# Kernel tuning notes

Measured on AMD Instinct MI355X. Metric: run time of the kernel, lower is better.

The kernel has to match this reference:

```python
import jax, jax.numpy as jnp
import numpy as np

B, Q, C, G = 16, 2000, 80, 100
COST_CLASS, COST_BBOX, COST_GIOU = 2.0, 5.0, 2.0
ALPHA, GAMMA = 0.25, 2.0
OTA_K = 5
CENTER_RADIUS = 2.5
MAX_ITERS = 1000  # safety cap on the (normally rarely-entered) rescue while-loop


def cxcywh_to_xyxy(b):
    cx, cy, w, h = jnp.split(b, 4, axis=-1)
    return jnp.concatenate([cx - 0.5 * w, cy - 0.5 * h, cx + 0.5 * w, cy + 0.5 * h], -1)


def xyxy_to_cxcywh(b):
    x1, y1, x2, y2 = jnp.split(b, 4, axis=-1)
    return jnp.concatenate([(x1 + x2) * 0.5, (y1 + y2) * 0.5, x2 - x1, y2 - y1], -1)


def box_iou(a, b):
    # a: [Q,4], b: [G,4] xyxy -> iou [Q,G], union [Q,G]
    area_a = (a[:, 2] - a[:, 0]) * (a[:, 3] - a[:, 1])
    area_b = (b[:, 2] - b[:, 0]) * (b[:, 3] - b[:, 1])
    lt = jnp.maximum(a[:, None, :2], b[None, :, :2])
    rb = jnp.minimum(a[:, None, 2:], b[None, :, 2:])
    wh = jnp.clip(rb - lt, 0.0)
    inter = wh[..., 0] * wh[..., 1]
    union = area_a[:, None] + area_b[None, :] - inter
    return inter / union, union


def generalized_box_iou(a, b):
    iou, union = box_iou(a, b)
    lt = jnp.minimum(a[:, None, :2], b[None, :, :2])
    rb = jnp.maximum(a[:, None, 2:], b[None, :, 2:])
    wh = jnp.clip(rb - lt, 0.0)
    area = wh[..., 0] * wh[..., 1]
    return iou - (area - union) / area


def get_in_boxes_info(boxes_c, tgt_c):
    # boxes_c: [Q,4] cxcywh (abs), tgt_c: [G,4] cxcywh (abs)
    xy = cxcywh_to_xyxy(tgt_c)  # [G,4]
    ax = boxes_c[:, 0:1]  # [Q,1]
    ay = boxes_c[:, 1:2]
    in_box = (ax > xy[:, 0][None, :]) & (ax < xy[:, 2][None, :]) & \
             (ay > xy[:, 1][None, :]) & (ay < xy[:, 3][None, :])  # [Q,G]
    w = xy[:, 2] - xy[:, 0]
    h = xy[:, 3] - xy[:, 1]
    in_ctr = (ax > (tgt_c[:, 0] - CENTER_RADIUS * w)[None, :]) & \
             (ax < (tgt_c[:, 0] + CENTER_RADIUS * w)[None, :]) & \
             (ay > (tgt_c[:, 1] - CENTER_RADIUS * h)[None, :]) & \
             (ay < (tgt_c[:, 1] + CENTER_RADIUS * h)[None, :])
    fg_mask = in_box.any(1) | in_ctr.any(1)  # [Q]
    return fg_mask, in_box & in_ctr


def dynamic_k_matching(cost, ious):
    # cost, ious: [Q,G]
    topk_ious, _ = jax.lax.top_k(ious.T, OTA_K)  # [G,k]
    dyn_k = jnp.clip(topk_ious.sum(1).astype(jnp.int32), 1, None)  # [G], <= OTA_K
    # rank of each query within each gt column (ascending cost, stable ties)
    ranks = jnp.argsort(jnp.argsort(cost, axis=0), axis=0)
    M = (ranks < dyn_k[None, :]).astype(cost.dtype)  # topk(largest=False) per column

    onehot = lambda idx: jax.nn.one_hot(idx, G, dtype=cost.dtype)
    # resolve anchors matched to >1 gt: keep the min-cost gt
    conflict0 = M.sum(1) > 1  # stale mask reused inside the while loop (faithful to torch code)
    M = jnp.where(conflict0[:, None], onehot(jnp.argmin(cost, axis=1)), M)

    qidx = jnp.arange(Q)

    def cond(state):
        M, cost, it = state
        return ((M.sum(0) == 0).any()) & (it < MAX_ITERS)

    def body(state):
        M, cost, it = state
        matched = M.sum(1) > 0
        cost = cost + 100000.0 * matched[:, None].astype(cost.dtype)
        unmatched_gt = M.sum(0) == 0  # [G]
        pos = jnp.argmin(cost, axis=0)  # [G] best anchor per gt (same cost for all, as in torch)
        add = unmatched_gt[None, :] & (qidx[:, None] == pos[None, :])
        M = jnp.where(add, jnp.asarray(1.0, cost.dtype), M)
        has_conf = (M.sum(1) > 1).any()
        M = jnp.where((has_conf & conflict0)[:, None], onehot(jnp.argmin(cost, axis=1)), M)
        return M, cost, it + 1

    M, cost, _ = jax.lax.while_loop(cond, body, (M, cost, jnp.int32(0)))

    selected = M.sum(1) > 0  # [Q] bool
    gt_idx = jnp.argmax(M, axis=1).astype(jnp.int32)  # [Q] (valid where selected)
    cost_m = jnp.where(M == 0, jnp.asarray(1e30, cost.dtype), cost)
    matched_qid = jnp.argmin(cost_m, axis=0).astype(jnp.int32)  # [G]
    return selected, gt_idx, matched_qid, M


def _match_one(logits, boxes, gtb, labels, img):
    # logits [Q,C], boxes [Q,4] cxcywh, gtb [G,4] cxcywh norm, labels [G] int, img [4]
    prob = jax.nn.sigmoid(logits)
    boxes_abs = cxcywh_to_xyxy(boxes) * img
    gt_abs = cxcywh_to_xyxy(gtb) * img
    fg_mask, in_bc = get_in_boxes_info(xyxy_to_cxcywh(boxes_abs), xyxy_to_cxcywh(gt_abs))
    ious, _ = box_iou(boxes_abs, gt_abs)
    neg = (1.0 - ALPHA) * prob ** GAMMA * (-jnp.log(1.0 - prob + 1e-8))
    pos = ALPHA * (1.0 - prob) ** GAMMA * (-jnp.log(prob + 1e-8))
    cost_class = (pos - neg)[:, labels]  # [Q,G]
    cost_bbox = jnp.sum(jnp.abs(boxes_abs[:, None, :] / img - gt_abs[None, :, :] / img), -1)
    cost_giou = -generalized_box_iou(boxes_abs, gt_abs)
    cost = (COST_BBOX * cost_bbox + COST_CLASS * cost_class + COST_GIOU * cost_giou
            + 100.0 * (~in_bc).astype(cost_bbox.dtype)
            + 10000.0 * (~fg_mask)[:, None].astype(cost_bbox.dtype))
    return dynamic_k_matching(cost, ious)


def setup_inputs() -> dict:
    key = jax.random.key(0)
    k1, k2, k3, k4 = jax.random.split(key, 4)
    return {
        "pred_logits": jax.random.normal(k1, (B, Q, C), dtype=jnp.float32),
        "pred_boxes": jax.random.uniform(k2, (B, Q, 4), dtype=jnp.float32),
        "gt_boxes": jax.random.uniform(k3, (B, G, 4), dtype=jnp.float32),
        "labels": jax.random.randint(k4, (B, G), 0, C),
        "image_size_xyxy": jnp.ones((B, 4), dtype=jnp.float32),
    }


def reference(pred_logits, pred_boxes, gt_boxes, labels, image_size_xyxy):
    selected, gt_idx, matched_qid, M = jax.vmap(_match_one)(
        pred_logits, pred_boxes, gt_boxes, labels, image_size_xyxy)
    # selected [B,Q] bool, gt_idx [B,Q] int32, matched_qid [B,G] int32, M [B,Q,G] float
    return selected, gt_idx, matched_qid, M
```

## Files before the change

kernel.cpp:

```cpp
#include <hip/hip_runtime.h>
#include <stdint.h>

#define BATCH 16
#define NQ 2000
#define NC 80
#define NG 100
#define MAX_ITERS 1000
#define MAXC 96
#define QT 32
#define TILES 63
#define K1_BLOCKS (BATCH * TILES)
#define K3_BS 1024
#define NW3 16
#define NCAND 8
#define LSTRIDE 9
#define QINF 0x7fffffff
#define SQINF 0x7fff

#define OFF_SEL 0
#define OFF_GTI (BATCH * NQ)
#define OFF_MQ (2 * BATCH * NQ)
#define OFF_M (2 * BATCH * NQ + BATCH * NG)

#define WS_LISTS 0
#define WS_MW    65536
#define WS_MIT   (WS_MW + 512000)
#define WS_CIDX  (WS_MIT + 64000)
#define WS_CROW  (WS_CIDX + 64000)
#define WS_SCAL  (WS_CROW + 614400)
#define WS_NEED  (WS_SCAL + 512)

__device__ __forceinline__ float fmut(float c, int k) {
    for (int i = 0; i < k; ++i) c += 100000.0f;
    return c;
}

__device__ __forceinline__ bool lexlt(float v1, int i1, float v2, int i2) {
    return (v1 < v2) | ((v1 == v2) & (i1 < i2));
}

#define CE(vv, ii, a, b) do { \
    bool t_ = lexlt(vv[b], ii[b], vv[a], ii[a]); \
    float lo_ = t_ ? vv[b] : vv[a]; float hi_ = t_ ? vv[a] : vv[b]; \
    int loi_ = t_ ? ii[b] : ii[a]; int hii_ = t_ ? ii[a] : ii[b]; \
    vv[a] = lo_; vv[b] = hi_; ii[a] = loi_; ii[b] = hii_; \
} while (0)

#define INS8(vv, ii, val, idx) do { float v_ = (val); int i_ = (idx); \
    bool ins_ = lexlt(v_, i_, vv[7], ii[7]); \
    vv[7] = ins_ ? v_ : vv[7]; ii[7] = ins_ ? i_ : ii[7]; \
    CE(vv, ii, 6, 7); CE(vv, ii, 5, 6); CE(vv, ii, 4, 5); CE(vv, ii, 3, 4); \
    CE(vv, ii, 2, 3); CE(vv, ii, 1, 2); CE(vv, ii, 0, 1); \
} while (0)

#define MERGE8(va, ia) do { \
    for (int off_ = 1; off_ < 64; off_ <<= 1) { \
        float bv_[8]; int bi_[8]; \
        _Pragma("unroll") \
        for (int j_ = 0; j_ < 8; ++j_) { bv_[j_] = __shfl_xor(va[j_], off_, 64); bi_[j_] = __shfl_xor(ia[j_], off_, 64); } \
        float mv_[8]; int mi_[8]; \
        _Pragma("unroll") \
        for (int j_ = 0; j_ < 8; ++j_) { \
            bool t_ = lexlt(bv_[7 - j_], bi_[7 - j_], va[j_], ia[j_]); \
            mv_[j_] = t_ ? bv_[7 - j_] : va[j_]; mi_[j_] = t_ ? bi_[7 - j_] : ia[j_]; \
        } \
        _Pragma("unroll") \
        for (int d_ = 4; d_ >= 1; d_ >>= 1) { \
            _Pragma("unroll") \
            for (int i_ = 0; i_ < 8; ++i_) { \
                if ((i_ & d_) == 0) CE(mv_, mi_, i_, (i_ | d_)); \
            } \
        } \
        _Pragma("unroll") \
        for (int j_ = 0; j_ < 8; ++j_) { va[j_] = mv_[j_]; ia[j_] = mi_[j_]; } \
    } \
} while (0)

__global__ __launch_bounds__(256) void fgcost_kernel(
    const float* __restrict__ logits, const float* __restrict__ pred_boxes,
    const float* __restrict__ gt_boxes, const int* __restrict__ labels,
    const float* __restrict__ img_sz, float* __restrict__ costT_all,
    float* __restrict__ rowamin) {
    const int tid = threadIdx.x;
    const int b = blockIdx.x / TILES;
    const int tile = blockIdx.x - b * TILES;
    const int q0 = tile * QT;

    __shared__ float ct[QT][NG + 1];
    __shared__ float s_rx1[NG], s_ry1[NG], s_rx2[NG], s_ry2[NG];
    __shared__ float s_clx[NG], s_chx[NG], s_cly[NG], s_chy[NG];
    __shared__ float s_gx1[NG], s_gy1[NG], s_gx2[NG], s_gy2[NG];
    __shared__ float s_d1[NG], s_d2[NG], s_d3[NG], s_d4[NG];
    __shared__ float s_ga[NG];
    __shared__ int s_lab[NG];
    __shared__ float pbx[QT][11];
    __shared__ unsigned fgm[QT];

    const float i0 = img_sz[b * 4 + 0], i1 = img_sz[b * 4 + 1];
    const float i2 = img_sz[b * 4 + 2], i3 = img_sz[b * 4 + 3];

    if (tid < NG) {
        const float4 gt = *reinterpret_cast<const float4*>(gt_boxes + (b * NG + tid) * 4);
        float GX1 = (gt.x - 0.5f * gt.z) * i0, GY1 = (gt.y - 0.5f * gt.w) * i1;
        float GX2 = (gt.x + 0.5f * gt.z) * i2, GY2 = (gt.y + 0.5f * gt.w) * i3;
        float tcx = (GX1 + GX2) * 0.5f, tcy = (GY1 + GY2) * 0.5f;
        float tw = GX2 - GX1, th = GY2 - GY1;
        float X1 = tcx - 0.5f * tw, Y1 = tcy - 0.5f * th;
        float X2 = tcx + 0.5f * tw, Y2 = tcy + 0.5f * th;
        float w_ = X2 - X1, h_ = Y2 - Y1;
        s_rx1[tid] = X1; s_ry1[tid] = Y1; s_rx2[tid] = X2; s_ry2[tid] = Y2;
        s_clx[tid] = tcx - 2.5f * w_; s_chx[tid] = tcx + 2.5f * w_;
        s_cly[tid] = tcy - 2.5f * h_; s_chy[tid] = tcy + 2.5f * h_;
        s_gx1[tid] = GX1; s_gy1[tid] = GY1; s_gx2[tid] = GX2; s_gy2[tid] = GY2;
        s_d1[tid] = GX1 / i0; s_d2[tid] = GY1 / i1; s_d3[tid] = GX2 / i2; s_d4[tid] = GY2 / i3;
        s_ga[tid] = (GX2 - GX1) * (GY2 - GY1);
        s_lab[tid] = labels[b * NG + tid];
    }
    if (tid < QT) {
        fgm[tid] = 0;
        int q = q0 + tid;
        if (q < NQ) {
            const float4 pb = *reinterpret_cast<const float4*>(pred_boxes + (size_t)(b * NQ + q) * 4);
            float x1 = (pb.x - 0.5f * pb.z) * i0, y1 = (pb.y - 0.5f * pb.w) * i1;
            float x2 = (pb.x + 0.5f * pb.z) * i2, y2 = (pb.y + 0.5f * pb.w) * i3;
            pbx[tid][0] = x1; pbx[tid][1] = y1; pbx[tid][2] = x2; pbx[tid][3] = y2;
            pbx[tid][4] = (x1 + x2) * 0.5f; pbx[tid][5] = (y1 + y2) * 0.5f;
            pbx[tid][6] = x1 / i0; pbx[tid][7] = y1 / i1; pbx[tid][8] = x2 / i2; pbx[tid][9] = y2 / i3;
            pbx[tid][10] = (x2 - x1) * (y2 - y1);
        }
    }
    __syncthreads();

    {
        int ql = tid & 31, part = tid >> 5;
        if (q0 + ql < NQ) {
            float ax = pbx[ql][4], ay = pbx[ql][5];
            int gbeg = part * 13;
            int gend = gbeg + 13 < NG ? gbeg + 13 : NG;
            bool any = false;
            for (int g = gbeg; g < gend; ++g) {
                bool in_box = (ax > s_rx1[g]) && (ax < s_rx2[g]) && (ay > s_ry1[g]) && (ay < s_ry2[g]);
                bool in_ctr = (ax > s_clx[g]) && (ax < s_chx[g]) && (ay > s_cly[g]) && (ay < s_chy[g]);
                any = any || in_box || in_ctr;
            }
            if (any) atomicOr(&fgm[ql], 1u);
        }
    }
    __syncthreads();

    for (int idx = tid; idx < QT * NG; idx += 256) {
        int ql = idx / NG, g = idx - ql * NG;
        int q = q0 + ql;
        if (q < NQ) {
            float x1 = pbx[ql][0], y1 = pbx[ql][1], x2 = pbx[ql][2], y2 = pbx[ql][3];
            float ax = pbx[ql][4], ay = pbx[ql][5];
            bool in_box = (ax > s_rx1[g]) && (ax < s_rx2[g]) && (ay > s_ry1[g]) && (ay < s_ry2[g]);
            bool in_ctr = (ax > s_clx[g]) && (ax < s_chx[g]) && (ay > s_cly[g]) && (ay < s_chy[g]);
            bool in_bc = in_box && in_ctr;
            bool fgb = fgm[ql] != 0;

            float lg = logits[(size_t)(b * NQ + q) * NC + s_lab[g]];
            float p = 1.0f / (1.0f + expf(-lg));
            float neg = 0.75f * (p * p) * (-logf(1.0f - p + 1e-8f));
            float pos = 0.25f * ((1.0f - p) * (1.0f - p)) * (-logf(p + 1e-8f));
            float cc = pos - neg;

            float cb = fabsf(pbx[ql][6] - s_d1[g]);
            cb = cb + fabsf(pbx[ql][7] - s_d2[g]);
            cb = cb + fabsf(pbx[ql][8] - s_d3[g]);
            cb = cb + fabsf(pbx[ql][9] - s_d4[g]);

            float aA = pbx[ql][10];
            float GX1 = s_gx1[g], GY1 = s_gy1[g], GX2 = s_gx2[g], GY2 = s_gy2[g];
            float lx = fmaxf(x1, GX1), ly = fmaxf(y1, GY1);
            float rx = fminf(x2, GX2), ry = fminf(y2, GY2);
            float iw = fmaxf(rx - lx, 0.0f), ih = fmaxf(ry - ly, 0.0f);
            float inter = iw * ih;
            float uni = aA + s_ga[g] - inter;
            float iou = inter / uni;
            float hx1 = fminf(x1, GX1), hy1 = fminf(y1, GY1);
            float hx2 = fmaxf(x2, GX2), hy2 = fmaxf(y2, GY2);
            float hw = fmaxf(hx2 - hx1, 0.0f), hh = fmaxf(hy2 - hy1, 0.0f);
            float harea = hw * hh;
            float giou = iou - (harea - uni) / harea;

            float cost = 5.0f * cb;
            cost = cost + 2.0f * cc;
            cost = cost + 2.0f * (-giou);
            cost = cost + (in_bc ? 0.0f : 100.0f);
            cost = cost + (fgb ? 0.0f : 10000.0f);
            ct[ql][g] = cost;
        }
    }
    __syncthreads();

    float* dst = costT_all + (size_t)b * NQ * NG;
    for (int idx = tid; idx < QT * NG; idx += 256) {
        int g = idx >> 5, ql = idx & 31;
        int q = q0 + ql;
        if (q < NQ) dst[(size_t)g * NQ + q] = ct[ql][g];
    }
    if (tid < QT && q0 + tid < NQ) {
        float mv = ct[tid][0]; int mg = 0;
        for (int g = 1; g < NG; ++g) { float v = ct[tid][g]; if (v < mv) { mv = v; mg = g; } }
        rowamin[b * NQ + q0 + tid] = (float)mg;
    }
}

__global__ __launch_bounds__(256) void init_kernel(const float* __restrict__ pred_boxes,
                                                   const float* __restrict__ gt_boxes,
                                                   const float* __restrict__ img_sz,
                                                   const float* __restrict__ costT_all,
                                                   float* __restrict__ lists) {
    const int tid = threadIdx.x;
    const int wid = tid >> 6, lane = tid & 63;

    if (blockIdx.x < 400) {
        int w = blockIdx.x * 4 + wid;
        int b = w / NG, g = w - b * NG;
        const float* col = costT_all + (size_t)b * NQ * NG + (size_t)g * NQ;

        float va[8]; int ia[8];
#pragma unroll
        for (int j = 0; j < 8; ++j) { va[j] = INFINITY; ia[j] = QINF; }
        for (int q = lane; q < NQ; q += 64) {
            float v = col[q];
            INS8(va, ia, v, q);
        }
        MERGE8(va, ia);
        if (lane == 0) {
            float* o = lists + (size_t)w * LSTRIDE;
            o[1] = (float)ia[0]; o[2] = (float)ia[1]; o[3] = (float)ia[2]; o[4] = (float)ia[3];
            o[5] = (float)ia[4]; o[6] = (float)ia[5]; o[7] = (float)ia[6]; o[8] = (float)ia[7];
        }
        return;
    }

    int w = (blockIdx.x - 400) * 4 + wid;
    int b = w / NG, g = w - b * NG;

    const float i0 = img_sz[b * 4 + 0], i1 = img_sz[b * 4 + 1];
    const float i2 = img_sz[b * 4 + 2], i3 = img_sz[b * 4 + 3];
    const float4 gt = *reinterpret_cast<const float4*>(gt_boxes + (b * NG + g) * 4);
    float GX1 = (gt.x - 0.5f * gt.z) * i0, GY1 = (gt.y - 0.5f * gt.w) * i1;
    float GX2 = (gt.x + 0.5f * gt.z) * i2, GY2 = (gt.y + 0.5f * gt.w) * i3;
    float GA = (GX2 - GX1) * (GY2 - GY1);

    const float* pbox = pred_boxes + (size_t)b * NQ * 4;
    float tv[5]; int ti[5];
#pragma unroll
    for (int j = 0; j < 5; ++j) { tv[j] = INFINITY; ti[j] = QINF; }

    for (int q = lane; q < NQ; q += 64) {
        const float4 pb = *reinterpret_cast<const float4*>(pbox + q * 4);
        float x1 = (pb.x - 0.5f * pb.z) * i0, y1 = (pb.y - 0.5f * pb.w) * i1;
        float x2 = (pb.x + 0.5f * pb.z) * i2, y2 = (pb.y + 0.5f * pb.w) * i3;
        float aA = (x2 - x1) * (y2 - y1);
        float lx = fmaxf(x1, GX1), ly = fmaxf(y1, GY1);
        float rx = fminf(x2, GX2), ry = fminf(y2, GY2);
        float iw = fmaxf(rx - lx, 0.0f), ih = fmaxf(ry - ly, 0.0f);
        float inter = iw * ih;
        float uni = aA + GA - inter;
        float niou = -(inter / uni);
        bool ins = lexlt(niou, q, tv[4], ti[4]);
        tv[4] = ins ? niou : tv[4]; ti[4] = ins ? q : ti[4];
        CE(tv, ti, 3, 4); CE(tv, ti, 2, 3); CE(tv, ti, 1, 2); CE(tv, ti, 0, 1);
    }

#pragma unroll
    for (int off = 1; off < 64; off <<= 1) {
        float bv[5]; int bi[5];
#pragma unroll
        for (int j = 0; j < 5; ++j) { bv[j] = __shfl_xor(tv[j], off, 64); bi[j] = __shfl_xor(ti[j], off, 64); }
        float mv[8]; int mi[8];
#pragma unroll
        for (int j = 0; j < 3; ++j) { mv[j] = tv[j]; mi[j] = ti[j]; }
#pragma unroll
        for (int j = 3; j < 5; ++j) {
            bool t = lexlt(bv[7 - j], bi[7 - j], tv[j], ti[j]);
            mv[j] = t ? bv[7 - j] : tv[j]; mi[j] = t ? bi[7 - j] : ti[j];
        }
#pragma unroll
        for (int j = 5; j < 8; ++j) { mv[j] = bv[7 - j]; mi[j] = bi[7 - j]; }
#pragma unroll
        for (int d = 4; d >= 1; d >>= 1) {
#pragma unroll
            for (int i = 0; i < 8; ++i) {
                if ((i & d) == 0) CE(mv, mi, i, (i | d));
            }
        }
#pragma unroll
        for (int j = 0; j < 5; ++j) { tv[j] = mv[j]; ti[j] = mi[j]; }
    }

    if (lane == 0) {
        float s = -((((tv[0] + tv[1]) + tv[2]) + tv[3]) + tv[4]);
        int k = (int)s;
        if (k < 1) k = 1;
        lists[(size_t)w * LSTRIDE] = (float)k;
    }
}

__global__ __launch_bounds__(K3_BS) void match_main(const float* __restrict__ lists,
                                                    const float* __restrict__ rowamin_all,
                                                    const float* __restrict__ costT_all,
                                                    char* __restrict__ ws) {
    const int b = blockIdx.x;
    const int tid = threadIdx.x;
    const int wave = tid >> 6;
    const int lane = tid & 63;

    __shared__ uint32_t Mw[4][NQ];
    __shared__ float crow[MAXC][NG + 1];
    __shared__ int m_it[NQ];
    __shared__ int16_t c16[NQ];
    __shared__ int16_t cand[NG][NCAND];
    __shared__ int crowq[MAXC];
    __shared__ int colcnt[NG];
    __shared__ int needscan[NG];
    __shared__ int touched[128];
    __shared__ int nconf0, nscan, ntq, persist;

    uint32_t* MwG = (uint32_t*)(ws + WS_MW) + (size_t)b * 4 * NQ;
    int16_t* mitG = (int16_t*)(ws + WS_MIT) + (size_t)b * NQ;
    int16_t* cidxG = (int16_t*)(ws + WS_CIDX) + (size_t)b * NQ;
    float* crowG = (float*)(ws + WS_CROW) + (size_t)b * MAXC * NG;
    int* scalG = (int*)(ws + WS_SCAL) + b * 8;
    const float* costT = costT_all + (size_t)b * NQ * NG;
    const float* rowamin_b = rowamin_all + b * NQ;

    if (tid == 0) { nconf0 = 0; nscan = 0; ntq = 0; persist = 0; }
    for (int q = tid; q < NQ; q += K3_BS) {
        Mw[0][q] = 0; Mw[1][q] = 0; Mw[2][q] = 0; Mw[3][q] = 0;
        c16[q] = -1; m_it[q] = QINF;
    }
    __syncthreads();

    if (tid < NG) {
        const float* o = lists + (size_t)(b * NG + tid) * LSTRIDE;
        int k = (int)o[0];
        int word = tid >> 5;
        uint32_t bit = 1u << (tid & 31);
        for (int j = 0; j < NCAND; ++j) {
            float f = o[1 + j];
            cand[tid][j] = (f >= 32767.0f) ? (int16_t)SQINF : (int16_t)(int)f;
        }
        for (int j = 0; j < 5; ++j)
            if (j < k) atomicOr(&Mw[word][(int)o[1 + j]], bit);
        colcnt[tid] = k;
    }
    __syncthreads();

    for (int q = tid; q < NQ; q += K3_BS) {
        uint32_t w0 = Mw[0][q], w1 = Mw[1][q], w2 = Mw[2][q], w3 = Mw[3][q];
        int pc = __popc(w0) + __popc(w1) + __popc(w2) + __popc(w3);
        if (pc > 1) {
            int slot = atomicAdd(&nconf0, 1);
            int c = (slot < MAXC) ? slot : -1;
            c16[q] = (c >= 0) ? (int16_t)c : (int16_t)-2;
            m_it[q] = -1;
            if (c >= 0) crowq[c] = q;
            int mg = (int)rowamin_b[q];
            uint32_t words[4] = {w0, w1, w2, w3};
            for (int w = 0; w < 4; ++w) {
                uint32_t word = words[w];
                while (word) {
                    int bp = __ffs(word) - 1;
                    word &= word - 1;
                    atomicSub(&colcnt[w * 32 + bp], 1);
                }
                Mw[w][q] = 0;
            }
            Mw[mg >> 5][q] = 1u << (mg & 31);
            atomicAdd(&colcnt[mg], 1);
        } else if (pc == 1) {
            m_it[q] = -1;
        }
    }
    __syncthreads();

    const int nc0 = nconf0;
    const int ncached = (nc0 < MAXC) ? nc0 : MAXC;
    const bool hasOvf = nc0 > MAXC;
    for (int i = tid; i < ncached * NG; i += K3_BS) {
        int c = i / NG, g = i - c * NG;
        crow[c][g] = costT[(size_t)g * NQ + crowq[c]];
    }
    __syncthreads();

    int unm = __syncthreads_or(tid < NG && colcnt[tid] == 0);
    int L = 0;

    for (int it = 0; it < MAX_ITERS; ++it) {
        if (!unm) break;
        L = it + 1;

        for (int i = tid; i < ncached * NG; i += K3_BS) {
            int c = i / NG, g = i - c * NG;
            crow[c][g] += 100000.0f;
        }
        if (tid < NG && colcnt[tid] == 0) {
            int g = tid;
            int win = -1;
            for (int j = 0; j < NCAND; ++j) {
                int qi = cand[g][j];
                if (qi != SQINF && m_it[qi] >= it) { win = qi; break; }
            }
            if (win >= 0) {
                atomicOr(&Mw[g >> 5][win], 1u << (g & 31));
                atomicMin(&m_it[win], it);
                colcnt[g] = 1;
                touched[atomicAdd(&ntq, 1)] = win;
            } else {
                needscan[atomicAdd(&nscan, 1)] = g;
            }
        }
        __syncthreads();

        int ns = nscan;
        if (ns > 0) {
            for (int s = wave; s < ns; s += NW3) {
                int g = needscan[s];
                const float* col = costT + (size_t)g * NQ;
                float mv = INFINITY; int mi = QINF;
                for (int q = lane; q < NQ; q += 64) {
                    if (m_it[q] >= it) {
                        float v = col[q];
                        if (v < mv || (v == mv && q < mi)) { mv = v; mi = q; }
                    }
                }
                for (int off = 1; off < 64; off <<= 1) {
                    float ov = __shfl_xor(mv, off); int oi = __shfl_xor(mi, off);
                    if (ov < mv || (ov == mv && oi < mi)) { mv = ov; mi = oi; }
                }
                if (mi == QINF) {
                    for (int q = lane; q < NQ; q += 64) {
                        int nq = it - m_it[q]; if (nq < 0) nq = 0;
                        float v = fmut(col[q], nq);
                        if (v < mv || (v == mv && q < mi)) { mv = v; mi = q; }
                    }
                    for (int off = 1; off < 64; off <<= 1) {
                        float ov = __shfl_xor(mv, off); int oi = __shfl_xor(mi, off);
                        if (ov < mv || (ov == mv && oi < mi)) { mv = ov; mi = oi; }
                    }
                }
                if (lane == 0) {
                    atomicOr(&Mw[g >> 5][mi], 1u << (g & 31));
                    atomicMin(&m_it[mi], it);
                    colcnt[g] = 1;
                    touched[atomicAdd(&ntq, 1)] = mi;
                }
            }
            __syncthreads();
        }

        int myconf = (tid == 0 && persist) ? 1 : 0;
        int nt = ntq;
        for (int s = tid; s < nt; s += K3_BS) {
            int q = touched[s];
            int pc = __popc(Mw[0][q]) + __popc(Mw[1][q]) + __popc(Mw[2][q]) + __popc(Mw[3][q]);
            if (pc > 1) {
                myconf = 1;
                if (c16[q] == -1) persist = 1;
            }
        }
        int hc = __syncthreads_or(myconf);
        if (!hc) break;

        if (tid == 0) { ntq = 0; nscan = 0; }
        for (int c = tid; c < ncached; c += K3_BS) {
            int q = crowq[c];
            float mv = crow[c][0]; int mg = 0;
            for (int g = 1; g < NG; ++g) { float v = crow[c][g]; if (v < mv) { mv = v; mg = g; } }
            int keepw = mg >> 5;
            uint32_t keepb = 1u << (mg & 31);
            for (int w = 0; w < 4; ++w) {
                uint32_t word = Mw[w][q];
                uint32_t keep = (w == keepw) ? keepb : 0u;
                uint32_t toclear = word & ~keep;
                while (toclear) {
                    int bp = __ffs(toclear) - 1;
                    toclear &= toclear - 1;
                    atomicSub(&colcnt[w * 32 + bp], 1);
                }
                if (keep && !(word & keep)) atomicAdd(&colcnt[mg], 1);
                Mw[w][q] = keep;
            }
        }
        if (hasOvf) {
            for (int q = tid; q < NQ; q += K3_BS) {
                if (c16[q] != -2) continue;
                int k = it + 1;
                float mv = fmut(costT[q], k); int mg = 0;
                for (int g = 1; g < NG; ++g) {
                    float v = fmut(costT[(size_t)g * NQ + q], k);
                    if (v < mv) { mv = v; mg = g; }
                }
                int keepw = mg >> 5;
                uint32_t keepb = 1u << (mg & 31);
                for (int w = 0; w < 4; ++w) {
                    uint32_t word = Mw[w][q];
                    uint32_t keep = (w == keepw) ? keepb : 0u;
                    uint32_t toclear = word & ~keep;
                    while (toclear) {
                        int bp = __ffs(toclear) - 1;
                        toclear &= toclear - 1;
                        atomicSub(&colcnt[w * 32 + bp], 1);
                    }
                    if (keep && !(word & keep)) atomicAdd(&colcnt[mg], 1);
                    Mw[w][q] = keep;
                }
            }
        }
        __syncthreads();
        unm = __syncthreads_or(tid < NG && colcnt[tid] == 0);
    }

    uint32_t* MwF = &Mw[0][0];
    for (int i = tid; i < 4 * NQ; i += K3_BS) MwG[i] = MwF[i];
    for (int q = tid; q < NQ; q += K3_BS) {
        int v = m_it[q];
        mitG[q] = (v > 32000) ? (int16_t)SQINF : (int16_t)v;
        cidxG[q] = c16[q];
    }
    for (int i = tid; i < ncached * NG; i += K3_BS) crowG[i] = crow[i / NG][i - (i / NG) * NG];
    if (tid == 0) { scalG[0] = nc0; scalG[1] = L; }
}

__global__ __launch_bounds__(256) void finish_kernel(const char* __restrict__ ws,
                                                     const float* __restrict__ costT_all,
                                                     float* __restrict__ out) {
    const int tid = threadIdx.x;
    const int blk = blockIdx.x;

    if (blk < 400) {
        int w = blk * 4 + (tid >> 6);
        int lane = tid & 63;
        int b = w / NG, g = w - b * NG;
        const int* scalG = (const int*)(ws + WS_SCAL) + b * 8;
        const int L = scalG[1];
        const uint32_t* MwP = (const uint32_t*)(ws + WS_MW) + (size_t)b * 4 * NQ + (size_t)(g >> 5) * NQ;
        const int16_t* mitG = (const int16_t*)(ws + WS_MIT) + (size_t)b * NQ;
        const int16_t* cidxG = (const int16_t*)(ws + WS_CIDX) + (size_t)b * NQ;
        const float* crowG = (const float*)(ws + WS_CROW) + (size_t)b * MAXC * NG;
        const float* col = costT_all + (size_t)b * NQ * NG + (size_t)g * NQ;
        const uint32_t bit = 1u << (g & 31);

        float mv = INFINITY; int mi = QINF;
        for (int q = lane; q < NQ; q += 64) {
            float v = 1e30f;
            if (MwP[q] & bit) {
                int c = cidxG[q];
                if (c >= 0) v = crowG[c * NG + g];
                else {
                    int m = mitG[q];
                    int nq = (m == SQINF) ? 0 : (L - 1 - m);
                    if (nq < 0) nq = 0;
                    v = fmut(col[q], nq);
                }
            }
            if (v < mv || (v == mv && q < mi)) { mv = v; mi = q; }
        }
        for (int off = 1; off < 64; off <<= 1) {
            float ov = __shfl_xor(mv, off); int oi = __shfl_xor(mi, off);
            if (ov < mv || (ov == mv && oi < mi)) { mv = ov; mi = oi; }
        }
        if (lane == 0) out[OFF_MQ + b * NG + g] = (float)mi;
        return;
    }

    int idx = (blk - 400) * 256 + tid;
    if (idx < BATCH * NQ) {
        int b = idx / NQ, q = idx - b * NQ;
        const uint32_t* MwG = (const uint32_t*)(ws + WS_MW) + (size_t)b * 4 * NQ;
        uint32_t w0 = MwG[q], w1 = MwG[NQ + q], w2 = MwG[2 * NQ + q], w3 = MwG[3 * NQ + q];
        out[OFF_SEL + idx] = (w0 | w1 | w2 | w3) ? 1.0f : 0.0f;
        int gi = 0;
        if (w0) gi = __ffs(w0) - 1;
        else if (w1) gi = 32 + __ffs(w1) - 1;
        else if (w2) gi = 64 + __ffs(w2) - 1;
        else if (w3) gi = 96 + __ffs(w3) - 1;
        out[OFF_GTI + idx] = (float)gi;
    }
}

__global__ __launch_bounds__(256) void expand_kernel(const char* __restrict__ ws,
                                                     float* __restrict__ outM) {
    const int blk = blockIdx.x;
    const int b = blk >> 3, j = blk & 7;
    const int q0 = j * 250;
    __shared__ uint32_t msk[4][256];
    const uint32_t* MwG = (const uint32_t*)(ws + WS_MW) + (size_t)b * 4 * NQ;
    for (int i = threadIdx.x; i < 1000; i += 256) {
        int w = i / 250, q = i - w * 250;
        msk[w][q] = MwG[w * NQ + q0 + q];
    }
    __syncthreads();
    float4* dst = reinterpret_cast<float4*>(outM + (size_t)b * NQ * NG + (size_t)q0 * NG);
    for (int i = threadIdx.x; i < 6250; i += 256) {
        int flat = i * 4;
        int ql = flat / NG;
        int g0 = flat - ql * NG;
        uint32_t w = msk[g0 >> 5][ql];
        int sh = g0 & 31;
        float4 v;
        v.x = ((w >> sh) & 1) ? 1.0f : 0.0f;
        v.y = ((w >> (sh + 1)) & 1) ? 1.0f : 0.0f;
        v.z = ((w >> (sh + 2)) & 1) ? 1.0f : 0.0f;
        v.w = ((w >> (sh + 3)) & 1) ? 1.0f : 0.0f;
        dst[i] = v;
    }
}

__global__ __launch_bounds__(K3_BS) void match_mono(const float* __restrict__ lists,
                                                    float* __restrict__ out) {
    const int b = blockIdx.x;
    const int tid = threadIdx.x;
    const int wave = tid >> 6;
    const int lane = tid & 63;

    __shared__ uint32_t Msh[NQ][4];
    __shared__ float crow[MAXC][NG + 1];
    __shared__ int m_it[NQ];
    __shared__ int16_t cidx[NQ];
    __shared__ int candq[NG][NCAND];
    __shared__ int crowq[MAXC];
    __shared__ int colcnt[NG];
    __shared__ int needscan[NG];
    __shared__ int touched[128];
    __shared__ int nconf0, nscan, ntq, persist;

    float* costT = out + OFF_M + (size_t)b * NQ * NG;
    float* selOut = out + OFF_SEL + b * NQ;
    float* gtiOut = out + OFF_GTI + b * NQ;
    const float* rowamin_b = out + OFF_GTI + b * NQ;
    float* mqOut = out + OFF_MQ + b * NG;

    if (tid == 0) { nconf0 = 0; nscan = 0; ntq = 0; persist = 0; }
    for (int q = tid; q < NQ; q += K3_BS) {
        Msh[q][0] = 0; Msh[q][1] = 0; Msh[q][2] = 0; Msh[q][3] = 0;
        cidx[q] = -1; m_it[q] = QINF;
    }
    __syncthreads();
    if (tid < NG) {
        const float* o = lists + (size_t)(b * NG + tid) * LSTRIDE;
        int k = (int)o[0];
        int word = tid >> 5;
        uint32_t bit = 1u << (tid & 31);
        for (int j = 0; j < NCAND; ++j) candq[tid][j] = (int)o[1 + j];
        for (int j = 0; j < 5; ++j)
            if (j < k) atomicOr(&Msh[candq[tid][j]][word], bit);
        colcnt[tid] = k;
    }
    __syncthreads();
    for (int q = tid; q < NQ; q += K3_BS) {
        uint4 m = *reinterpret_cast<const uint4*>(&Msh[q][0]);
        int pc = __popc(m.x) + __popc(m.y) + __popc(m.z) + __popc(m.w);
        if (pc > 1) {
            int slot = atomicAdd(&nconf0, 1);
            int c = (slot < MAXC) ? slot : -1;
            cidx[q] = (c >= 0) ? (int16_t)c : (int16_t)-2;
            m_it[q] = -1;
            if (c >= 0) crowq[c] = q;
            int mg = (int)rowamin_b[q];
            uint32_t words[4] = {m.x, m.y, m.z, m.w};
            for (int w = 0; w < 4; ++w) {
                uint32_t word = words[w];
                while (word) {
                    int bp = __ffs(word) - 1;
                    word &= word - 1;
                    atomicSub(&colcnt[w * 32 + bp], 1);
                }
                Msh[q][w] = 0;
            }
            Msh[q][mg >> 5] = 1u << (mg & 31);
            atomicAdd(&colcnt[mg], 1);
        } else if (pc == 1) {
            m_it[q] = -1;
        }
    }
    __syncthreads();
    const int ncached = (nconf0 < MAXC) ? nconf0 : MAXC;
    const bool hasOvf = nconf0 > MAXC;
    for (int i = tid; i < ncached * NG; i += K3_BS) {
        int c = i / NG, g = i - c * NG;
        crow[c][g] = costT[(size_t)g * NQ + crowq[c]];
    }
    __syncthreads();
    int unm = __syncthreads_or(tid < NG && colcnt[tid] == 0);
    int L = 0;
    for (int it = 0; it < MAX_ITERS; ++it) {
        if (!unm) break;
        L = it + 1;
        for (int i = tid; i < ncached * NG; i += K3_BS) {
            int c = i / NG, g = i - c * NG;
            crow[c][g] += 100000.0f;
        }
        if (tid < NG && colcnt[tid] == 0) {
            int g = tid;
            int win = -1;
            for (int j = 0; j < NCAND; ++j) {
                int qi = candq[g][j];
                if (qi != QINF && m_it[qi] >= it) { win = qi; break; }
            }
            if (win >= 0) {
                atomicOr(&Msh[win][g >> 5], 1u << (g & 31));
                atomicMin(&m_it[win], it);
                colcnt[g] = 1;
                touched[atomicAdd(&ntq, 1)] = win;
            } else {
                needscan[atomicAdd(&nscan, 1)] = g;
            }
        }
        __syncthreads();
        int ns = nscan;
        if (ns > 0) {
            for (int s = wave; s < ns; s += NW3) {
                int g = needscan[s];
                const float* col = costT + (size_t)g * NQ;
                float mv = INFINITY; int mi = QINF;
                for (int q = lane; q < NQ; q += 64) {
                    if (m_it[q] >= it) {
                        float v = col[q];
                        if (v < mv || (v == mv && q < mi)) { mv = v; mi = q; }
                    }
                }
                for (int off = 1; off < 64; off <<= 1) {
                    float ov = __shfl_xor(mv, off); int oi = __shfl_xor(mi, off);
                    if (ov < mv || (ov == mv && oi < mi)) { mv = ov; mi = oi; }
                }
                if (mi == QINF) {
                    for (int q = lane; q < NQ; q += 64) {
                        int nq = it - m_it[q]; if (nq < 0) nq = 0;
                        float v = fmut(col[q], nq);
                        if (v < mv || (v == mv && q < mi)) { mv = v; mi = q; }
                    }
                    for (int off = 1; off < 64; off <<= 1) {
                        float ov = __shfl_xor(mv, off); int oi = __shfl_xor(mi, off);
                        if (ov < mv || (ov == mv && oi < mi)) { mv = ov; mi = oi; }
                    }
                }
                if (lane == 0) {
                    atomicOr(&Msh[mi][g >> 5], 1u << (g & 31));
                    atomicMin(&m_it[mi], it);
                    colcnt[g] = 1;
                    touched[atomicAdd(&ntq, 1)] = mi;
                }
            }
            __syncthreads();
        }
        int myconf = (tid == 0 && persist) ? 1 : 0;
        int nt = ntq;
        for (int s = tid; s < nt; s += K3_BS) {
            int q = touched[s];
            uint4 m = *reinterpret_cast<const uint4*>(&Msh[q][0]);
            int pc = __popc(m.x) + __popc(m.y) + __popc(m.z) + __popc(m.w);
            if (pc > 1) {
                myconf = 1;
                if (cidx[q] == -1) persist = 1;
            }
        }
        int hc = __syncthreads_or(myconf);
        if (!hc) break;
        if (tid == 0) { ntq = 0; nscan = 0; }
        for (int c = tid; c < ncached; c += K3_BS) {
            int q = crowq[c];
            float mv = crow[c][0]; int mg = 0;
            for (int g = 1; g < NG; ++g) { float v = crow[c][g]; if (v < mv) { mv = v; mg = g; } }
            int keepw = mg >> 5;
            uint32_t keepb = 1u << (mg & 31);
            for (int w = 0; w < 4; ++w) {
                uint32_t word = Msh[q][w];
                uint32_t keep = (w == keepw) ? keepb : 0u;
                uint32_t toclear = word & ~keep;
                while (toclear) {
                    int bp = __ffs(toclear) - 1;
                    toclear &= toclear - 1;
                    atomicSub(&colcnt[w * 32 + bp], 1);
                }
                if (keep && !(word & keep)) atomicAdd(&colcnt[mg], 1);
                Msh[q][w] = keep;
            }
        }
        if (hasOvf) {
            for (int q = tid; q < NQ; q += K3_BS) {
                if (cidx[q] != -2) continue;
                int k = it + 1;
                float mv = fmut(costT[q], k); int mg = 0;
                for (int g = 1; g < NG; ++g) {
                    float v = fmut(costT[(size_t)g * NQ + q], k);
                    if (v < mv) { mv = v; mg = g; }
                }
                int keepw = mg >> 5;
                uint32_t keepb = 1u << (mg & 31);
                for (int w = 0; w < 4; ++w) {
                    uint32_t word = Msh[q][w];
                    uint32_t keep = (w == keepw) ? keepb : 0u;
                    uint32_t toclear = word & ~keep;
                    while (toclear) {
                        int bp = __ffs(toclear) - 1;
                        toclear &= toclear - 1;
                        atomicSub(&colcnt[w * 32 + bp], 1);
                    }
                    if (keep && !(word & keep)) atomicAdd(&colcnt[mg], 1);
                    Msh[q][w] = keep;
                }
            }
        }
        __syncthreads();
        unm = __syncthreads_or(tid < NG && colcnt[tid] == 0);
    }
    for (int g = wave; g < NG; g += NW3) {
        int word = g >> 5;
        uint32_t bit = 1u << (g & 31);
        const float* col = costT + (size_t)g * NQ;
        float mv = INFINITY; int mi = QINF;
        for (int q = lane; q < NQ; q += 64) {
            float v = 1e30f;
            if (Msh[q][word] & bit) {
                int c = cidx[q];
                if (c >= 0) v = crow[c][g];
                else {
                    int nq = L - 1 - m_it[q]; if (nq < 0) nq = 0;
                    v = fmut(col[q], nq);
                }
            }
            if (v < mv || (v == mv && q < mi)) { mv = v; mi = q; }
        }
        for (int off = 1; off < 64; off <<= 1) {
            float ov = __shfl_xor(mv, off); int oi = __shfl_xor(mi, off);
            if (ov < mv || (ov == mv && oi < mi)) { mv = ov; mi = oi; }
        }
        if (lane == 0) mqOut[g] = (float)mi;
    }
    for (int q = tid; q < NQ; q += K3_BS) {
        uint4 m = *reinterpret_cast<const uint4*>(&Msh[q][0]);
        selOut[q] = (m.x | m.y | m.z | m.w) ? 1.0f : 0.0f;
        int gi = 0;
        if (m.x) gi = __ffs(m.x) - 1;
        else if (m.y) gi = 32 + __ffs(m.y) - 1;
        else if (m.z) gi = 64 + __ffs(m.z) - 1;
        else if (m.w) gi = 96 + __ffs(m.w) - 1;
        gtiOut[q] = (float)gi;
    }
    __syncthreads();
    for (int i = tid; i < NQ * NG; i += K3_BS) {
        int q = i / NG;
        int g = i - q * NG;
        costT[i] = (Msh[q][g >> 5] & (1u << (g & 31))) ? 1.0f : 0.0f;
    }
}

extern "C" void kernel_launch(void* const* d_in, const int* in_sizes, int n_in,
                              void* d_out, int out_size, void* d_ws, size_t ws_size,
                              hipStream_t stream) {
    const float* logits = (const float*)d_in[0];
    const float* pboxes = (const float*)d_in[1];
    const float* gboxes = (const float*)d_in[2];
    const int* labels = (const int*)d_in[3];
    const float* img = (const float*)d_in[4];
    float* out = (float*)d_out;
    char* ws = (char*)d_ws;
    float* lists = (float*)(ws + WS_LISTS);

    fgcost_kernel<<<K1_BLOCKS, 256, 0, stream>>>(logits, pboxes, gboxes, labels, img,
                                                 out + OFF_M, out + OFF_GTI);
    init_kernel<<<800, 256, 0, stream>>>(pboxes, gboxes, img, out + OFF_M, lists);

    if (ws_size >= (size_t)WS_NEED) {
        match_main<<<BATCH, K3_BS, 0, stream>>>(lists, out + OFF_GTI, out + OFF_M, ws);
        finish_kernel<<<525, 256, 0, stream>>>(ws, out + OFF_M, out);
        expand_kernel<<<BATCH * 8, 256, 0, stream>>>(ws, out + OFF_M);
    } else {
        match_mono<<<BATCH, K3_BS, 0, stream>>>(lists, out);
    }
}
```

Baseline: 88.62 us.

## Fuse dyn-k IoU top-k into cost kernel and merge finish/expand kernels

Moves the per-GT dynamic-k top-5 IoU computation out of init_kernel into extra blocks of fgcost_kernel, so it runs alongside the cost computation. init_kernel shrinks to the candidate-list part, and finish and expand are merged into one launch. The cost matrix now goes to a workspace buffer instead of the output M region, which removes the ordering dependency between expand writing M and reading cost. This cuts launch count and serialization, at the price of a roughly 12.8MB workspace requirement.

```diff
diff --git a/kernel.cpp b/kernel.cpp
--- a/kernel.cpp
+++ b/kernel.cpp
@@ -9,7 +9,8 @@
 #define MAXC 96
 #define QT 32
 #define TILES 63
-#define K1_BLOCKS (BATCH * TILES)
+#define K1_TILEB (BATCH * TILES)
+#define K1_BLOCKS (K1_TILEB + 400)
 #define K3_BS 1024
 #define NW3 16
 #define NCAND 8
@@ -22,13 +23,14 @@
 #define OFF_MQ (2 * BATCH * NQ)
 #define OFF_M (2 * BATCH * NQ + BATCH * NG)
 
-#define WS_LISTS 0
-#define WS_MW    65536
-#define WS_MIT   (WS_MW + 512000)
-#define WS_CIDX  (WS_MIT + 64000)
-#define WS_CROW  (WS_CIDX + 64000)
-#define WS_SCAL  (WS_CROW + 614400)
-#define WS_NEED  (WS_SCAL + 512)
+#define WS_COST  0
+#define WS_LISTS 12800000
+#define WS_MW    12864000
+#define WS_MIT   13376000
+#define WS_CIDX  13440000
+#define WS_CROW  13504000
+#define WS_SCAL  14118400
+#define WS_NEED  14118912
 
 __device__ __forceinline__ float fmut(float c, int k) {
     for (int i = 0; i < k; ++i) c += 100000.0f;
@@ -76,12 +78,87 @@
     } \
 } while (0)
 
+__device__ __forceinline__ void dynk_wave(int w, int lane,
+                                          const float* __restrict__ pred_boxes,
+                                          const float* __restrict__ gt_boxes,
+                                          const float* __restrict__ img_sz,
+                                          float* __restrict__ lists) {
+    int b = w / NG, g = w - b * NG;
+    const float i0 = img_sz[b * 4 + 0], i1 = img_sz[b * 4 + 1];
+    const float i2 = img_sz[b * 4 + 2], i3 = img_sz[b * 4 + 3];
+    const float4 gt = *reinterpret_cast<const float4*>(gt_boxes + (b * NG + g) * 4);
+    float GX1 = (gt.x - 0.5f * gt.z) * i0, GY1 = (gt.y - 0.5f * gt.w) * i1;
+    float GX2 = (gt.x + 0.5f * gt.z) * i2, GY2 = (gt.y + 0.5f * gt.w) * i3;
+    float GA = (GX2 - GX1) * (GY2 - GY1);
+
+    const float* pbox = pred_boxes + (size_t)b * NQ * 4;
+    float tv[5]; int ti[5];
+#pragma unroll
+    for (int j = 0; j < 5; ++j) { tv[j] = INFINITY; ti[j] = QINF; }
+
+    for (int q = lane; q < NQ; q += 64) {
+        const float4 pb = *reinterpret_cast<const float4*>(pbox + q * 4);
+        float x1 = (pb.x - 0.5f * pb.z) * i0, y1 = (pb.y - 0.5f * pb.w) * i1;
+        float x2 = (pb.x + 0.5f * pb.z) * i2, y2 = (pb.y + 0.5f * pb.w) * i3;
+        float aA = (x2 - x1) * (y2 - y1);
+        float lx = fmaxf(x1, GX1), ly = fmaxf(y1, GY1);
+        float rx = fminf(x2, GX2), ry = fminf(y2, GY2);
+        float iw = fmaxf(rx - lx, 0.0f), ih = fmaxf(ry - ly, 0.0f);
+        float inter = iw * ih;
+        float uni = aA + GA - inter;
+        float niou = -(inter / uni);
+        bool ins = lexlt(niou, q, tv[4], ti[4]);
+        tv[4] = ins ? niou : tv[4]; ti[4] = ins ? q : ti[4];
+        CE(tv, ti, 3, 4); CE(tv, ti, 2, 3); CE(tv, ti, 1, 2); CE(tv, ti, 0, 1);
+    }
+
+#pragma unroll
+    for (int off = 1; off < 64; off <<= 1) {
+        float bv[5]; int bi[5];
+#pragma unroll
+        for (int j = 0; j < 5; ++j) { bv[j] = __shfl_xor(tv[j], off, 64); bi[j] = __shfl_xor(ti[j], off, 64); }
+        float mv[8]; int mi[8];
+#pragma unroll
+        for (int j = 0; j < 3; ++j) { mv[j] = tv[j]; mi[j] = ti[j]; }
+#pragma unroll
+        for (int j = 3; j < 5; ++j) {
+            bool t = lexlt(bv[7 - j], bi[7 - j], tv[j], ti[j]);
+            mv[j] = t ? bv[7 - j] : tv[j]; mi[j] = t ? bi[7 - j] : ti[j];
+        }
+#pragma unroll
+        for (int j = 5; j < 8; ++j) { mv[j] = bv[7 - j]; mi[j] = bi[7 - j]; }
+#pragma unroll
+        for (int d = 4; d >= 1; d >>= 1) {
+#pragma unroll
+            for (int i = 0; i < 8; ++i) {
+                if ((i & d) == 0) CE(mv, mi, i, (i | d));
+            }
+        }
+#pragma unroll
+        for (int j = 0; j < 5; ++j) { tv[j] = mv[j]; ti[j] = mi[j]; }
+    }
+
+    if (lane == 0) {
+        float s = -((((tv[0] + tv[1]) + tv[2]) + tv[3]) + tv[4]);
+        int k = (int)s;
+        if (k < 1) k = 1;
+        lists[(size_t)w * LSTRIDE] = (float)k;
+    }
+}
+
 __global__ __launch_bounds__(256) void fgcost_kernel(
     const float* __restrict__ logits, const float* __restrict__ pred_boxes,
     const float* __restrict__ gt_boxes, const int* __restrict__ labels,
     const float* __restrict__ img_sz, float* __restrict__ costT_all,
-    float* __restrict__ rowamin) {
+    float* __restrict__ rowamin, float* __restrict__ lists) {
     const int tid = threadIdx.x;
+
+    if (blockIdx.x >= K1_TILEB) {
+        int w = (blockIdx.x - K1_TILEB) * 4 + (tid >> 6);
+        dynk_wave(w, tid & 63, pred_boxes, gt_boxes, img_sz, lists);
+        return;
+    }
+
     const int b = blockIdx.x / TILES;
     const int tile = blockIdx.x - b * TILES;
     const int q0 = tile * QT;
@@ -237,68 +314,7 @@
     }
 
     int w = (blockIdx.x - 400) * 4 + wid;
-    int b = w / NG, g = w - b * NG;
-
-    const float i0 = img_sz[b * 4 + 0], i1 = img_sz[b * 4 + 1];
-    const float i2 = img_sz[b * 4 + 2], i3 = img_sz[b * 4 + 3];
-    const float4 gt = *reinterpret_cast<const float4*>(gt_boxes + (b * NG + g) * 4);
-    float GX1 = (gt.x - 0.5f * gt.z) * i0, GY1 = (gt.y - 0.5f * gt.w) * i1;
-    float GX2 = (gt.x + 0.5f * gt.z) * i2, GY2 = (gt.y + 0.5f * gt.w) * i3;
-    float GA = (GX2 - GX1) * (GY2 - GY1);
-
-    const float* pbox = pred_boxes + (size_t)b * NQ * 4;
-    float tv[5]; int ti[5];
-#pragma unroll
-    for (int j = 0; j < 5; ++j) { tv[j] = INFINITY; ti[j] = QINF; }
-
-    for (int q = lane; q < NQ; q += 64) {
-        const float4 pb = *reinterpret_cast<const float4*>(pbox + q * 4);
-        float x1 = (pb.x - 0.5f * pb.z) * i0, y1 = (pb.y - 0.5f * pb.w) * i1;
-        float x2 = (pb.x + 0.5f * pb.z) * i2, y2 = (pb.y + 0.5f * pb.w) * i3;
-        float aA = (x2 - x1) * (y2 - y1);
-        float lx = fmaxf(x1, GX1), ly = fmaxf(y1, GY1);
-        float rx = fminf(x2, GX2), ry = fminf(y2, GY2);
-        float iw = fmaxf(rx - lx, 0.0f), ih = fmaxf(ry - ly, 0.0f);
-        float inter = iw * ih;
-        float uni = aA + GA - inter;
-        float niou = -(inter / uni);
-        bool ins = lexlt(niou, q, tv[4], ti[4]);
-        tv[4] = ins ? niou : tv[4]; ti[4] = ins ? q : ti[4];
-        CE(tv, ti, 3, 4); CE(tv, ti, 2, 3); CE(tv, ti, 1, 2); CE(tv, ti, 0, 1);
-    }
-
-#pragma unroll
-    for (int off = 1; off < 64; off <<= 1) {
-        float bv[5]; int bi[5];
-#pragma unroll
-        for (int j = 0; j < 5; ++j) { bv[j] = __shfl_xor(tv[j], off, 64); bi[j] = __shfl_xor(ti[j], off, 64); }
-        float mv[8]; int mi[8];
-#pragma unroll
-        for (int j = 0; j < 3; ++j) { mv[j] = tv[j]; mi[j] = ti[j]; }
-#pragma unroll
-        for (int j = 3; j < 5; ++j) {
-            bool t = lexlt(bv[7 - j], bi[7 - j], tv[j], ti[j]);
-            mv[j] = t ? bv[7 - j] : tv[j]; mi[j] = t ? bi[7 - j] : ti[j];
-        }
-#pragma unroll
-        for (int j = 5; j < 8; ++j) { mv[j] = bv[7 - j]; mi[j] = bi[7 - j]; }
-#pragma unroll
-        for (int d = 4; d >= 1; d >>= 1) {
-#pragma unroll
-            for (int i = 0; i < 8; ++i) {
-                if ((i & d) == 0) CE(mv, mi, i, (i | d));
-            }
-        }
-#pragma unroll
-        for (int j = 0; j < 5; ++j) { tv[j] = mv[j]; ti[j] = mi[j]; }
-    }
-
-    if (lane == 0) {
-        float s = -((((tv[0] + tv[1]) + tv[2]) + tv[3]) + tv[4]);
-        int k = (int)s;
-        if (k < 1) k = 1;
-        lists[(size_t)w * LSTRIDE] = (float)k;
-    }
+    dynk_wave(w, lane, pred_boxes, gt_boxes, img_sz, lists);
 }
 
 __global__ __launch_bounds__(K3_BS) void match_main(const float* __restrict__ lists,
@@ -527,9 +543,9 @@
     if (tid == 0) { scalG[0] = nc0; scalG[1] = L; }
 }
 
-__global__ __launch_bounds__(256) void finish_kernel(const char* __restrict__ ws,
-                                                     const float* __restrict__ costT_all,
-                                                     float* __restrict__ out) {
+__global__ __launch_bounds__(256) void finish_ex(const char* __restrict__ ws,
+                                                 const float* __restrict__ costT_all,
+                                                 float* __restrict__ out) {
     const int tid = threadIdx.x;
     const int blk = blockIdx.x;
 
@@ -569,35 +585,35 @@
         return;
     }
 
-    int idx = (blk - 400) * 256 + tid;
-    if (idx < BATCH * NQ) {
-        int b = idx / NQ, q = idx - b * NQ;
-        const uint32_t* MwG = (const uint32_t*)(ws + WS_MW) + (size_t)b * 4 * NQ;
-        uint32_t w0 = MwG[q], w1 = MwG[NQ + q], w2 = MwG[2 * NQ + q], w3 = MwG[3 * NQ + q];
-        out[OFF_SEL + idx] = (w0 | w1 | w2 | w3) ? 1.0f : 0.0f;
-        int gi = 0;
-        if (w0) gi = __ffs(w0) - 1;
-        else if (w1) gi = 32 + __ffs(w1) - 1;
-        else if (w2) gi = 64 + __ffs(w2) - 1;
-        else if (w3) gi = 96 + __ffs(w3) - 1;
-        out[OFF_GTI + idx] = (float)gi;
-    }
-}
-
-__global__ __launch_bounds__(256) void expand_kernel(const char* __restrict__ ws,
-                                                     float* __restrict__ outM) {
-    const int blk = blockIdx.x;
-    const int b = blk >> 3, j = blk & 7;
+    if (blk < 525) {
+        int idx = (blk - 400) * 256 + tid;
+        if (idx < BATCH * NQ) {
+            int b = idx / NQ, q = idx - b * NQ;
+            const uint32_t* MwG = (const uint32_t*)(ws + WS_MW) + (size_t)b * 4 * NQ;
+            uint32_t w0 = MwG[q], w1 = MwG[NQ + q], w2 = MwG[2 * NQ + q], w3 = MwG[3 * NQ + q];
+            out[OFF_SEL + idx] = (w0 | w1 | w2 | w3) ? 1.0f : 0.0f;
+            int gi = 0;
+            if (w0) gi = __ffs(w0) - 1;
+            else if (w1) gi = 32 + __ffs(w1) - 1;
+            else if (w2) gi = 64 + __ffs(w2) - 1;
+            else if (w3) gi = 96 + __ffs(w3) - 1;
+            out[OFF_GTI + idx] = (float)gi;
+        }
+        return;
+    }
+
+    const int e = blk - 525;
+    const int b = e >> 3, j = e & 7;
     const int q0 = j * 250;
     __shared__ uint32_t msk[4][256];
     const uint32_t* MwG = (const uint32_t*)(ws + WS_MW) + (size_t)b * 4 * NQ;
-    for (int i = threadIdx.x; i < 1000; i += 256) {
+    for (int i = tid; i < 1000; i += 256) {
         int w = i / 250, q = i - w * 250;
         msk[w][q] = MwG[w * NQ + q0 + q];
     }
     __syncthreads();
-    float4* dst = reinterpret_cast<float4*>(outM + (size_t)b * NQ * NG + (size_t)q0 * NG);
-    for (int i = threadIdx.x; i < 6250; i += 256) {
+    float4* dst = reinterpret_cast<float4*>(out + OFF_M + (size_t)b * NQ * NG + (size_t)q0 * NG);
+    for (int i = tid; i < 6250; i += 256) {
         int flat = i * 4;
         int ql = flat / NG;
         int g0 = flat - ql * NG;
@@ -861,17 +877,20 @@
     const float* img = (const float*)d_in[4];
     float* out = (float*)d_out;
     char* ws = (char*)d_ws;
-    float* lists = (float*)(ws + WS_LISTS);
-
-    fgcost_kernel<<<K1_BLOCKS, 256, 0, stream>>>(logits, pboxes, gboxes, labels, img,
-                                                 out + OFF_M, out + OFF_GTI);
-    init_kernel<<<800, 256, 0, stream>>>(pboxes, gboxes, img, out + OFF_M, lists);
 
     if (ws_size >= (size_t)WS_NEED) {
-        match_main<<<BATCH, K3_BS, 0, stream>>>(lists, out + OFF_GTI, out + OFF_M, ws);
-        finish_kernel<<<525, 256, 0, stream>>>(ws, out + OFF_M, out);
-        expand_kernel<<<BATCH * 8, 256, 0, stream>>>(ws, out + OFF_M);
+        float* costT = (float*)(ws + WS_COST);
+        float* lists = (float*)(ws + WS_LISTS);
+        fgcost_kernel<<<K1_BLOCKS, 256, 0, stream>>>(logits, pboxes, gboxes, labels, img,
+                                                     costT, out + OFF_GTI, lists);
+        init_kernel<<<400, 256, 0, stream>>>(pboxes, gboxes, img, costT, lists);
+        match_main<<<BATCH, K3_BS, 0, stream>>>(lists, out + OFF_GTI, costT, ws);
+        finish_ex<<<653, 256, 0, stream>>>(ws, costT, out);
     } else {
+        float* lists = (float*)ws;
+        fgcost_kernel<<<K1_TILEB, 256, 0, stream>>>(logits, pboxes, gboxes, labels, img,
+                                                    out + OFF_M, out + OFF_GTI, lists);
+        init_kernel<<<800, 256, 0, stream>>>(pboxes, gboxes, img, out + OFF_M, lists);
         match_mono<<<BATCH, K3_BS, 0, stream>>>(lists, out);
     }
 }
```

After: 84.45 us, median of 2. -4.7%, faster.
